# Performance work log

Measured on AMD Instinct MI355X. Metric: run time of the kernel, lower is better.

The kernel has to match this reference:

```python
import jax, jax.numpy as jnp
import numpy as np

DIM = 1024
N_HEADS = 16
HD = DIM // N_HEADS
EPS = 1.1920928955078125e-07  # torch.finfo(float32).eps, F.rms_norm default


def apply_rotary(x, cos, sin):
    # x: (B,T,H,hd); cos/sin: (1,T,1,hd//2)
    d = x.shape[-1] // 2
    x1, x2 = x[..., :d], x[..., d:]
    return jnp.concatenate([x1 * cos + x2 * sin, -x1 * sin + x2 * cos], axis=-1)


def rms_norm(x):
    ms = jnp.mean(jnp.square(x), axis=-1, keepdims=True)
    return x * jax.lax.rsqrt(ms + EPS)


def setup_inputs() -> dict:
    key = jax.random.key(0)
    ks = jax.random.split(key, 7)
    B, T = 4, 4096
    x = jax.random.normal(ks[0], (B, T, DIM), dtype=jnp.float32)
    # rotary angles
    theta = jax.random.uniform(ks[1], (1, T, 1, HD // 2), dtype=jnp.float32) * (2 * np.pi)
    cos, sin = jnp.cos(theta), jnp.sin(theta)
    s = 1.0 / np.sqrt(DIM)
    wq = jax.random.normal(ks[2], (DIM, DIM), dtype=jnp.float32) * s
    wk = jax.random.normal(ks[3], (DIM, DIM), dtype=jnp.float32) * s
    wv = jax.random.normal(ks[4], (DIM, DIM), dtype=jnp.float32) * s
    wo = jax.random.normal(ks[5], (DIM, DIM), dtype=jnp.float32) * s
    return {"x": x, "cos": cos, "sin": sin, "wq": wq, "wk": wk, "wv": wv, "wo": wo}


def reference(x, cos, sin, wq, wk, wv, wo):
    B, T, _ = x.shape
    # fused-style QKV projections (Linear: x @ W.T), reshape to heads
    q = (x @ wq.T).reshape(B, T, N_HEADS, HD)
    k = (x @ wk.T).reshape(B, T, N_HEADS, HD)
    v = (x @ wv.T).reshape(B, T, N_HEADS, HD)
    q = rms_norm(apply_rotary(q, cos, sin))
    k = rms_norm(apply_rotary(k, cos, sin))
    # SDPA, non-causal, scale = 1/sqrt(hd)
    scores = jnp.einsum("bqhd,bkhd->bhqk", q, k) * (1.0 / np.sqrt(HD))
    attn = jax.nn.softmax(scores, axis=-1)
    y = jnp.einsum("bhqk,bkhd->bqhd", attn, v).reshape(B, T, DIM)
    return y @ wo.T
```

## Files before the change

kernel.cpp:

```cpp
#include <hip/hip_runtime.h>
#include <cstdint>

#define DIMSZ 1024
#define NH 16
#define HDIM 64
#define TLEN 4096
#define BSZ 4
#define EPSF 1.1920928955078125e-07f

typedef __bf16 bf16x8 __attribute__((ext_vector_type(8)));
typedef float f32x4 __attribute__((ext_vector_type(4)));
typedef float f32x16 __attribute__((ext_vector_type(16)));
typedef uint16_t u16x8 __attribute__((ext_vector_type(8)));

__device__ __forceinline__ uint16_t f2bf(float f) {
  uint32_t u = __builtin_bit_cast(uint32_t, f);
  u += 0x7FFFu + ((u >> 16) & 1u);
  return (uint16_t)(u >> 16);
}
__device__ __forceinline__ float bf2f(uint16_t b) {
  return __builtin_bit_cast(float, ((uint32_t)b) << 16);
}

__device__ __forceinline__ void gl_lds16(const uint16_t* g, uint16_t* l) {
  __builtin_amdgcn_global_load_lds(
      (__attribute__((address_space(1))) uint32_t*)(g),
      (__attribute__((address_space(3))) uint32_t*)(l), 16, 0, 0);
}

__device__ __forceinline__ uint32_t cvtpk(float a, float b) {
  uint32_t r;
  asm volatile("v_cvt_pk_bf16_f32 %0, %1, %2" : "=v"(r) : "v"(a), "v"(b));
  return r;
}
__device__ __forceinline__ void pls32(uint32_t& a, uint32_t& b) {
  asm volatile("v_permlane32_swap_b32 %0, %1" : "+v"(a), "+v"(b));
}
__device__ __forceinline__ float pairmax32(float x) {
  return fmaxf(x, __shfl_xor(x, 32));
}
__device__ __forceinline__ float pairsum32(float x) {
  return x + __shfl_xor(x, 32);
}

__global__ __launch_bounds__(256) void cvt_f32_bf16(const float* __restrict__ src,
                                                    uint16_t* __restrict__ dst, int n8) {
  int i = blockIdx.x * 256 + threadIdx.x;
  if (i >= n8) return;
  const float4* s4 = ((const float4*)src) + (size_t)i * 2;
  float4 a = s4[0], b = s4[1];
  u16x8 o;
  o[0] = f2bf(a.x); o[1] = f2bf(a.y); o[2] = f2bf(a.z); o[3] = f2bf(a.w);
  o[4] = f2bf(b.x); o[5] = f2bf(b.y); o[6] = f2bf(b.z); o[7] = f2bf(b.w);
  *(((u16x8*)dst) + i) = o;
}

template <int EPI>
__global__ __launch_bounds__(256) void gemm_bt(const uint16_t* __restrict__ A,
                                               const uint16_t* __restrict__ Bw,
                                               float* __restrict__ C,
                                               uint16_t* __restrict__ q_out,
                                               uint16_t* __restrict__ k_out,
                                               uint16_t* __restrict__ v_out,
                                               int M, int N, int K) {
  __shared__ uint16_t As[128 * 32];
  __shared__ uint16_t Bs[128 * 32];
  const int nb = blockIdx.x, mb = blockIdx.y;
  const int tid = threadIdx.x;
  const int wave = tid >> 6, lane = tid & 63;
  const int l15 = lane & 15, l4 = lane >> 4;
  const int wr = wave >> 1, wc = wave & 1;

  f32x4 acc[4][4];
  const f32x4 fz = {0.f, 0.f, 0.f, 0.f};
#pragma unroll
  for (int i = 0; i < 4; ++i)
#pragma unroll
    for (int j = 0; j < 4; ++j) acc[i][j] = fz;

  const uint16_t* Ab = A + (size_t)mb * 128 * K;
  const uint16_t* Bb = Bw + (size_t)nb * 128 * K;
  const int rA = wave * 32 + (lane >> 2);
  const int cA = (lane & 3) * 8;

  for (int k0 = 0; k0 < K; k0 += 32) {
    gl_lds16(Ab + (size_t)rA * K + k0 + cA, &As[(wave * 32) * 32]);
    gl_lds16(Ab + (size_t)(rA + 16) * K + k0 + cA, &As[(wave * 32 + 16) * 32]);
    gl_lds16(Bb + (size_t)rA * K + k0 + cA, &Bs[(wave * 32) * 32]);
    gl_lds16(Bb + (size_t)(rA + 16) * K + k0 + cA, &Bs[(wave * 32 + 16) * 32]);
    __syncthreads();
    bf16x8 af[4], bfr[4];
#pragma unroll
    for (int i = 0; i < 4; ++i)
      af[i] = *(const bf16x8*)&As[(wr * 64 + i * 16 + l15) * 32 + l4 * 8];
#pragma unroll
    for (int j = 0; j < 4; ++j)
      bfr[j] = *(const bf16x8*)&Bs[(wc * 64 + j * 16 + l15) * 32 + l4 * 8];
#pragma unroll
    for (int i = 0; i < 4; ++i)
#pragma unroll
      for (int j = 0; j < 4; ++j)
        acc[i][j] = __builtin_amdgcn_mfma_f32_16x16x32_bf16(af[i], bfr[j], acc[i][j], 0, 0, 0);
    __syncthreads();
  }

  const int mrow = mb * 128 + wr * 64;
  const int ncol = nb * 128 + wc * 64;
  if (EPI == 0) {
#pragma unroll
    for (int i = 0; i < 4; ++i)
#pragma unroll
      for (int j = 0; j < 4; ++j) {
        int n = ncol + j * 16 + l15;
#pragma unroll
        for (int r = 0; r < 4; ++r) {
          int m = mrow + i * 16 + l4 * 4 + r;
          C[(size_t)m * N + n] = acc[i][j][r];
        }
      }
  } else {
#pragma unroll
    for (int i = 0; i < 4; ++i)
#pragma unroll
      for (int j = 0; j < 4; ++j) {
        int n = ncol + j * 16 + l15;
        int tens = n >> 10;
        int h = (n >> 6) & (NH - 1);
        int d = n & (HDIM - 1);
        uint16_t* dst = (tens == 0) ? q_out : ((tens == 1) ? k_out : v_out);
#pragma unroll
        for (int r = 0; r < 4; ++r) {
          int m = mrow + i * 16 + l4 * 4 + r;
          int b = m >> 12, t = m & (TLEN - 1);
          dst[((((size_t)b * NH + h) * TLEN) + t) * HDIM + d] = f2bf(acc[i][j][r]);
        }
      }
  }
}

__global__ __launch_bounds__(256) void rope_rms(uint16_t* __restrict__ qh,
                                                uint16_t* __restrict__ kh,
                                                const float* __restrict__ cosb,
                                                const float* __restrict__ sinb) {
  const int wid = blockIdx.x * 4 + (threadIdx.x >> 6);
  const int lane = threadIdx.x & 63;
  const int t = wid & (TLEN - 1);
  const int p = lane & 31;
  const float c = cosb[t * 32 + p];
  const float s = sinb[t * 32 + p];
  const size_t base = (size_t)wid * HDIM;
  {
    float v = bf2f(qh[base + lane]);
    float x1 = __shfl(v, p);
    float x2 = __shfl(v, p + 32);
    float rot = (lane < 32) ? (x1 * c + x2 * s) : (x2 * c - x1 * s);
    float ss = rot * rot;
#pragma unroll
    for (int off = 1; off < 64; off <<= 1) ss += __shfl_xor(ss, off);
    float sc = rsqrtf(ss * (1.0f / HDIM) + EPSF) * 0.125f;
    qh[base + lane] = f2bf(rot * sc);
  }
  {
    float v = bf2f(kh[base + lane]);
    float x1 = __shfl(v, p);
    float x2 = __shfl(v, p + 32);
    float rot = (lane < 32) ? (x1 * c + x2 * s) : (x2 * c - x1 * s);
    float ss = rot * rot;
#pragma unroll
    for (int off = 1; off < 64; off <<= 1) ss += __shfl_xor(ss, off);
    kh[base + lane] = f2bf(rot * rsqrtf(ss * (1.0f / HDIM) + EPSF));
  }
}

__global__ __launch_bounds__(256) void flash_attn(const uint16_t* __restrict__ qh,
                                                  const uint16_t* __restrict__ kh,
                                                  const uint16_t* __restrict__ vh,
                                                  uint16_t* __restrict__ yw) {
  __shared__ __align__(16) char smem_raw[18432];
  uint16_t* Ksm = (uint16_t*)smem_raw;
  uint16_t* Vsm = (uint16_t*)(smem_raw + 8192);

  const int braw = blockIdx.x;
  const int bid = (braw & 7) * 256 + (braw >> 3);
  const int qt = bid & 31;
  const int bh = bid >> 5;
  const int tid = threadIdx.x;
  const int wave = tid >> 6, lane = tid & 63;
  const int q5 = lane & 31, hi = lane >> 5;

  const uint16_t* qb = qh + ((size_t)bh * TLEN + qt * 128 + wave * 32) * HDIM;
  bf16x8 qf[4];
#pragma unroll
  for (int ks = 0; ks < 4; ++ks)
    qf[ks] = *(const bf16x8*)(qb + q5 * HDIM + ks * 16 + hi * 8);

  const uint16_t* kb = kh + (size_t)bh * TLEN * HDIM;
  const uint16_t* vb = vh + (size_t)bh * TLEN * HDIM;

  const int krow = wave * 16 + (lane >> 3);
  const int kc8 = (lane & 7) ^ (krow & 7);
  const size_t koff = (size_t)krow * HDIM + kc8 * 8;
  uint16_t* ks_dst = &Ksm[wave * 16 * 64];

  f32x16 accO[2];
  float m_run = -INFINITY, l_run = 0.f;
#pragma unroll
  for (int db = 0; db < 2; ++db)
#pragma unroll
    for (int r = 0; r < 16; ++r) accO[db][r] = 0.f;

  for (int kv0 = 0; kv0 < TLEN; kv0 += 64) {
    __syncthreads();
    gl_lds16(kb + (size_t)kv0 * HDIM + koff, ks_dst);
    gl_lds16(kb + (size_t)kv0 * HDIM + koff + 8 * HDIM, ks_dst + 8 * 64);
#pragma unroll
    for (int it = 0; it < 2; ++it) {
      int idx = tid + it * 256;
      int row = idx & 63, c8 = (idx >> 6) * 8;
      u16x8 vv = *(const u16x8*)(vb + (size_t)(kv0 + row) * HDIM + c8);
#pragma unroll
      for (int e = 0; e < 8; ++e) Vsm[(c8 + e) * 72 + row] = vv[e];
    }
    __syncthreads();

    f32x16 sA, sB;
#pragma unroll
    for (int r = 0; r < 16; ++r) { sA[r] = 0.f; sB[r] = 0.f; }
#pragma unroll
    for (int ks = 0; ks < 4; ++ks) {
      int cc = ((ks * 2 + hi) ^ (q5 & 7)) * 8;
      bf16x8 kf0 = *(const bf16x8*)&Ksm[q5 * 64 + cc];
      bf16x8 kf1 = *(const bf16x8*)&Ksm[(32 + q5) * 64 + cc];
      sA = __builtin_amdgcn_mfma_f32_32x32x16_bf16(kf0, qf[ks], sA, 0, 0, 0);
      sB = __builtin_amdgcn_mfma_f32_32x32x16_bf16(kf1, qf[ks], sB, 0, 0, 0);
    }

    float pm = sA[0];
#pragma unroll
    for (int r = 1; r < 16; ++r) pm = fmaxf(pm, sA[r]);
#pragma unroll
    for (int r = 0; r < 16; ++r) pm = fmaxf(pm, sB[r]);
    pm = pairmax32(pm);
    if (__any(pm > m_run + 8.0f)) {
      float mn = fmaxf(m_run, pm);
      float c = __expf(m_run - mn);
      m_run = mn;
      l_run *= c;
#pragma unroll
      for (int db = 0; db < 2; ++db)
#pragma unroll
        for (int r = 0; r < 16; ++r) accO[db][r] *= c;
    }
#pragma unroll
    for (int r = 0; r < 16; ++r) {
      sA[r] = __expf(sA[r] - m_run);
      sB[r] = __expf(sB[r] - m_run);
    }
    float sm = 0.f;
#pragma unroll
    for (int r = 0; r < 16; ++r) sm += sA[r] + sB[r];
    l_run += pairsum32(sm);

    bf16x8 pf[4];
    {
      uint32_t a0, a1, b0, b1;
      a0 = cvtpk(sA[0], sA[1]);  a1 = cvtpk(sA[2], sA[3]);
      b0 = cvtpk(sA[4], sA[5]);  b1 = cvtpk(sA[6], sA[7]);
      pls32(a0, b0); pls32(a1, b1);
      uint4 u = make_uint4(a0, a1, b0, b1);
      pf[0] = __builtin_bit_cast(bf16x8, u);
      a0 = cvtpk(sA[8], sA[9]);  a1 = cvtpk(sA[10], sA[11]);
      b0 = cvtpk(sA[12], sA[13]); b1 = cvtpk(sA[14], sA[15]);
      pls32(a0, b0); pls32(a1, b1);
      u = make_uint4(a0, a1, b0, b1);
      pf[1] = __builtin_bit_cast(bf16x8, u);
      a0 = cvtpk(sB[0], sB[1]);  a1 = cvtpk(sB[2], sB[3]);
      b0 = cvtpk(sB[4], sB[5]);  b1 = cvtpk(sB[6], sB[7]);
      pls32(a0, b0); pls32(a1, b1);
      u = make_uint4(a0, a1, b0, b1);
      pf[2] = __builtin_bit_cast(bf16x8, u);
      a0 = cvtpk(sB[8], sB[9]);  a1 = cvtpk(sB[10], sB[11]);
      b0 = cvtpk(sB[12], sB[13]); b1 = cvtpk(sB[14], sB[15]);
      pls32(a0, b0); pls32(a1, b1);
      u = make_uint4(a0, a1, b0, b1);
      pf[3] = __builtin_bit_cast(bf16x8, u);
    }

#pragma unroll
    for (int ksl = 0; ksl < 4; ++ksl) {
#pragma unroll
      for (int db = 0; db < 2; ++db) {
        bf16x8 vf = *(const bf16x8*)&Vsm[(db * 32 + q5) * 72 + ksl * 16 + hi * 8];
        accO[db] = __builtin_amdgcn_mfma_f32_32x32x16_bf16(vf, pf[ksl], accO[db], 0, 0, 0);
      }
    }
  }

  __syncthreads();
  uint16_t* Epi = (uint16_t*)smem_raw + wave * 2304;
  float inv = 1.0f / l_run;
#pragma unroll
  for (int db = 0; db < 2; ++db)
#pragma unroll
    for (int r = 0; r < 16; ++r) {
      int d = db * 32 + (r & 3) + 8 * (r >> 2) + 4 * hi;
      Epi[q5 * 72 + d] = f2bf(accO[db][r] * inv);
    }
  const int b = bh >> 4, h = bh & (NH - 1);
#pragma unroll
  for (int i = 0; i < 4; ++i) {
    int c = lane + i * 64;
    int row = c >> 3, off = (c & 7) * 8;
    u16x8 vv = *(const u16x8*)&Epi[row * 72 + off];
    int t = qt * 128 + wave * 32 + row;
    *(u16x8*)&yw[((size_t)b * TLEN + t) * DIMSZ + h * HDIM + off] = vv;
  }
}

extern "C" void kernel_launch(void* const* d_in, const int* in_sizes, int n_in,
                              void* d_out, int out_size, void* d_ws, size_t ws_size,
                              hipStream_t stream) {
  const float* x = (const float*)d_in[0];
  const float* cosb = (const float*)d_in[1];
  const float* sinb = (const float*)d_in[2];
  const float* wq = (const float*)d_in[3];
  const float* wk = (const float*)d_in[4];
  const float* wv = (const float*)d_in[5];
  const float* wo = (const float*)d_in[6];
  float* out = (float*)d_out;

  char* w = (char*)d_ws;
  uint16_t* qh = (uint16_t*)w;    w += (size_t)BSZ * NH * TLEN * HDIM * 2;
  uint16_t* kh = (uint16_t*)w;    w += (size_t)BSZ * NH * TLEN * HDIM * 2;
  uint16_t* vh = (uint16_t*)w;    w += (size_t)BSZ * NH * TLEN * HDIM * 2;
  uint16_t* xb = (uint16_t*)w;    w += (size_t)BSZ * TLEN * DIMSZ * 2;
  uint16_t* wqkvb = (uint16_t*)w; w += (size_t)3 * DIMSZ * DIMSZ * 2;
  uint16_t* wob = (uint16_t*)w;   w += (size_t)DIMSZ * DIMSZ * 2;

  cvt_f32_bf16<<<8192, 256, 0, stream>>>(x, xb, 2097152);
  cvt_f32_bf16<<<512, 256, 0, stream>>>(wq, wqkvb, 131072);
  cvt_f32_bf16<<<512, 256, 0, stream>>>(wk, wqkvb + DIMSZ * DIMSZ, 131072);
  cvt_f32_bf16<<<512, 256, 0, stream>>>(wv, wqkvb + 2 * DIMSZ * DIMSZ, 131072);
  cvt_f32_bf16<<<512, 256, 0, stream>>>(wo, wob, 131072);

  gemm_bt<1><<<dim3(24, 128), 256, 0, stream>>>(xb, wqkvb, nullptr, qh, kh, vh,
                                                BSZ * TLEN, 3 * DIMSZ, DIMSZ);
  rope_rms<<<65536, 256, 0, stream>>>(qh, kh, cosb, sinb);
  flash_attn<<<2048, 256, 0, stream>>>(qh, kh, vh, xb);
  gemm_bt<0><<<dim3(8, 128), 256, 0, stream>>>(xb, wob, out, nullptr, nullptr, nullptr,
                                               BSZ * TLEN, DIMSZ, DIMSZ);
}
```

Measured before the change: 799.2 us.

## Double-buffer K/V tiles in flash attention to overlap loads with compute

The flash attention loop now uses two LDS buffers for K and V. The next tile's K is issued via global_load_lds and its V is loaded into registers before the current tile's MFMAs, and V is transposed into the other buffer afterwards, so each iteration has one barrier instead of two. The row-sum shuffle across lane halves is also deferred to the epilogue, and the asm volatile markers are dropped so the compiler can schedule the cvt and permlane instructions. LDS use roughly doubles, which may reduce occupancy, and the extra live V registers add register pressure.

```diff
diff --git a/kernel.cpp b/kernel.cpp
--- a/kernel.cpp
+++ b/kernel.cpp
@@ -30,17 +30,14 @@
 
 __device__ __forceinline__ uint32_t cvtpk(float a, float b) {
   uint32_t r;
-  asm volatile("v_cvt_pk_bf16_f32 %0, %1, %2" : "=v"(r) : "v"(a), "v"(b));
+  asm("v_cvt_pk_bf16_f32 %0, %1, %2" : "=v"(r) : "v"(a), "v"(b));
   return r;
 }
 __device__ __forceinline__ void pls32(uint32_t& a, uint32_t& b) {
-  asm volatile("v_permlane32_swap_b32 %0, %1" : "+v"(a), "+v"(b));
+  asm("v_permlane32_swap_b32 %0, %1" : "+v"(a), "+v"(b));
 }
 __device__ __forceinline__ float pairmax32(float x) {
   return fmaxf(x, __shfl_xor(x, 32));
-}
-__device__ __forceinline__ float pairsum32(float x) {
-  return x + __shfl_xor(x, 32);
 }
 
 __global__ __launch_bounds__(256) void cvt_f32_bf16(const float* __restrict__ src,
@@ -176,9 +173,7 @@
                                                   const uint16_t* __restrict__ kh,
                                                   const uint16_t* __restrict__ vh,
                                                   uint16_t* __restrict__ yw) {
-  __shared__ __align__(16) char smem_raw[18432];
-  uint16_t* Ksm = (uint16_t*)smem_raw;
-  uint16_t* Vsm = (uint16_t*)(smem_raw + 8192);
+  __shared__ __align__(16) char smem[34816];
 
   const int braw = blockIdx.x;
   const int bid = (braw & 7) * 256 + (braw >> 3);
@@ -200,7 +195,10 @@
   const int krow = wave * 16 + (lane >> 3);
   const int kc8 = (lane & 7) ^ (krow & 7);
   const size_t koff = (size_t)krow * HDIM + kc8 * 8;
-  uint16_t* ks_dst = &Ksm[wave * 16 * 64];
+  const int kdst = wave * 16 * 64;
+
+  const int vrow = tid & 63;
+  const int vc8 = (tid >> 6) * 8;
 
   f32x16 accO[2];
   float m_run = -INFINITY, l_run = 0.f;
@@ -209,19 +207,35 @@
 #pragma unroll
     for (int r = 0; r < 16; ++r) accO[db][r] = 0.f;
 
-  for (int kv0 = 0; kv0 < TLEN; kv0 += 64) {
-    __syncthreads();
-    gl_lds16(kb + (size_t)kv0 * HDIM + koff, ks_dst);
-    gl_lds16(kb + (size_t)kv0 * HDIM + koff + 8 * HDIM, ks_dst + 8 * 64);
-#pragma unroll
-    for (int it = 0; it < 2; ++it) {
-      int idx = tid + it * 256;
-      int row = idx & 63, c8 = (idx >> 6) * 8;
-      u16x8 vv = *(const u16x8*)(vb + (size_t)(kv0 + row) * HDIM + c8);
-#pragma unroll
-      for (int e = 0; e < 8; ++e) Vsm[(c8 + e) * 72 + row] = vv[e];
-    }
-    __syncthreads();
+  gl_lds16(kb + koff, (uint16_t*)smem + kdst);
+  gl_lds16(kb + koff + 8 * HDIM, (uint16_t*)smem + kdst + 8 * 64);
+  {
+    const uint16_t* vsrc = vb + (size_t)vrow * HDIM + vc8;
+    u16x8 a = *(const u16x8*)vsrc;
+    u16x8 b2 = *(const u16x8*)(vsrc + 32);
+    uint16_t* V0 = (uint16_t*)(smem + 16384);
+#pragma unroll
+    for (int e = 0; e < 8; ++e) {
+      V0[(vc8 + e) * 72 + vrow] = a[e];
+      V0[(vc8 + 32 + e) * 72 + vrow] = b2[e];
+    }
+  }
+  __syncthreads();
+
+  for (int t = 0; t < 64; ++t) {
+    const int cur = t & 1;
+    const uint16_t* Kc = (const uint16_t*)(smem + cur * 8192);
+    const uint16_t* Vc = (const uint16_t*)(smem + 16384 + cur * 9216);
+    u16x8 va, vb2;
+    if (t < 63) {
+      const uint16_t* ksrc = kb + (size_t)(t + 1) * 64 * HDIM;
+      uint16_t* Kn = (uint16_t*)(smem + (cur ^ 1) * 8192);
+      gl_lds16(ksrc + koff, Kn + kdst);
+      gl_lds16(ksrc + koff + 8 * HDIM, Kn + kdst + 8 * 64);
+      const uint16_t* vsrc = vb + ((size_t)(t + 1) * 64 + vrow) * HDIM + vc8;
+      va = *(const u16x8*)vsrc;
+      vb2 = *(const u16x8*)(vsrc + 32);
+    }
 
     f32x16 sA, sB;
 #pragma unroll
@@ -229,8 +243,8 @@
 #pragma unroll
     for (int ks = 0; ks < 4; ++ks) {
       int cc = ((ks * 2 + hi) ^ (q5 & 7)) * 8;
-      bf16x8 kf0 = *(const bf16x8*)&Ksm[q5 * 64 + cc];
-      bf16x8 kf1 = *(const bf16x8*)&Ksm[(32 + q5) * 64 + cc];
+      bf16x8 kf0 = *(const bf16x8*)&Kc[q5 * 64 + cc];
+      bf16x8 kf1 = *(const bf16x8*)&Kc[(32 + q5) * 64 + cc];
       sA = __builtin_amdgcn_mfma_f32_32x32x16_bf16(kf0, qf[ks], sA, 0, 0, 0);
       sB = __builtin_amdgcn_mfma_f32_32x32x16_bf16(kf1, qf[ks], sB, 0, 0, 0);
     }
@@ -251,15 +265,15 @@
 #pragma unroll
         for (int r = 0; r < 16; ++r) accO[db][r] *= c;
     }
+    float lacc = 0.f;
 #pragma unroll
     for (int r = 0; r < 16; ++r) {
-      sA[r] = __expf(sA[r] - m_run);
-      sB[r] = __expf(sB[r] - m_run);
-    }
-    float sm = 0.f;
-#pragma unroll
-    for (int r = 0; r < 16; ++r) sm += sA[r] + sB[r];
-    l_run += pairsum32(sm);
+      float ea = __expf(sA[r] - m_run);
+      float eb = __expf(sB[r] - m_run);
+      sA[r] = ea; sB[r] = eb;
+      lacc += ea + eb;
+    }
+    l_run += lacc;
 
     bf16x8 pf[4];
     {
@@ -290,15 +304,26 @@
     for (int ksl = 0; ksl < 4; ++ksl) {
 #pragma unroll
       for (int db = 0; db < 2; ++db) {
-        bf16x8 vf = *(const bf16x8*)&Vsm[(db * 32 + q5) * 72 + ksl * 16 + hi * 8];
+        bf16x8 vf = *(const bf16x8*)&Vc[(db * 32 + q5) * 72 + ksl * 16 + hi * 8];
         accO[db] = __builtin_amdgcn_mfma_f32_32x32x16_bf16(vf, pf[ksl], accO[db], 0, 0, 0);
       }
     }
-  }
-
+
+    if (t < 63) {
+      uint16_t* Vn = (uint16_t*)(smem + 16384 + (cur ^ 1) * 9216);
+#pragma unroll
+      for (int e = 0; e < 8; ++e) {
+        Vn[(vc8 + e) * 72 + vrow] = va[e];
+        Vn[(vc8 + 32 + e) * 72 + vrow] = vb2[e];
+      }
+    }
+    __syncthreads();
+  }
+
+  float l_tot = l_run + __shfl_xor(l_run, 32);
+  float inv = 1.0f / l_tot;
   __syncthreads();
-  uint16_t* Epi = (uint16_t*)smem_raw + wave * 2304;
-  float inv = 1.0f / l_run;
+  uint16_t* Epi = (uint16_t*)smem + wave * 2304;
 #pragma unroll
   for (int db = 0; db < 2; ++db)
 #pragma unroll
```

Result: no change. 809.6 us (+1.3%).
